# Performance work log

Measured on AMD Instinct MI355X. Metric: run time of the kernel, lower is better.

The kernel has to match this reference:

```python
import jax, jax.numpy as jnp
import numpy as np

N_NODES = 100000


def gcn_conv(x, src, dst, deg_inv_sqrt, W, b):
    # x: [N, Fin], src/dst: [E_total] (self-loops included), W: [Fin, Fout]
    h = x @ W                                  # [N, Fout]
    norm = deg_inv_sqrt[src] * deg_inv_sqrt[dst]  # [E_total]
    msgs = h[src] * norm[:, None]              # [E_total, Fout] gather
    out = jax.ops.segment_sum(msgs, dst, num_segments=N_NODES)  # scatter-add
    return out + b


def setup_inputs() -> dict:
    key = jax.random.key(0)
    k1, k2, k3, k4, k5, k6, k7, k8 = jax.random.split(key, 8)
    input_dim, hidden_dim, out_dim = 4, 64, 2
    n_edges = 3200000
    x = jax.random.normal(k1, (N_NODES, input_dim), dtype=jnp.float32)
    edge_index = jax.random.randint(k2, (2, n_edges), 0, N_NODES, dtype=jnp.int64)
    s1 = 1.0 / np.sqrt(input_dim)
    s2 = 1.0 / np.sqrt(hidden_dim)
    W1 = jax.random.uniform(k3, (input_dim, hidden_dim), jnp.float32, -s1, s1)
    b1 = jnp.zeros((hidden_dim,), jnp.float32)
    W2 = jax.random.uniform(k4, (hidden_dim, hidden_dim), jnp.float32, -s2, s2)
    b2 = jnp.zeros((hidden_dim,), jnp.float32)
    Wf = jax.random.uniform(k5, (hidden_dim, out_dim), jnp.float32, -s2, s2)
    bf = jax.random.uniform(k6, (out_dim,), jnp.float32, -s2, s2)
    return {"x": x, "edge_index": edge_index, "W1": W1, "b1": b1,
            "W2": W2, "b2": b2, "Wf": Wf, "bf": bf}


def reference(x, edge_index, W1, b1, W2, b2, Wf, bf):
    # Add self-loops (PyG GCNConv default)
    loop = jnp.arange(N_NODES, dtype=edge_index.dtype)
    src = jnp.concatenate([edge_index[0], loop])
    dst = jnp.concatenate([edge_index[1], loop])
    # Symmetric normalization: degree on destination after self-loops
    deg = jax.ops.segment_sum(jnp.ones_like(dst, dtype=x.dtype), dst,
                              num_segments=N_NODES)
    deg_inv_sqrt = jnp.where(deg > 0, jax.lax.rsqrt(deg), 0.0)
    h = jax.nn.relu(gcn_conv(x, src, dst, deg_inv_sqrt, W1, b1))
    h = jax.nn.relu(gcn_conv(h, src, dst, deg_inv_sqrt, W2, b2))
    return h @ Wf + bf
```

## Files before the change

kernel.cpp:

```cpp
#include <hip/hip_runtime.h>
#include <hip/hip_bf16.h>

#define N_NODES 100000
#define N_EDGES 3200000
#define NB ((N_NODES + 255) / 256)
#define NBUCKET NB
#define EPB 8192
#define NPB ((N_EDGES + EPB - 1) / EPB)
#define BCAP 11264

__device__ inline unsigned f2bf(float f) {
  unsigned x = __float_as_uint(f);
  return (x + 0x7FFFu + ((x >> 16) & 1u)) >> 16;
}


__global__ void __launch_bounds__(256) k_pass1(const int* __restrict__ src,
                                               const int* __restrict__ dst,
                                               int* __restrict__ gcur,
                                               unsigned int* __restrict__ eb) {
  __shared__ int hist[NBUCKET];
  __shared__ int gbase[NBUCKET];
  int tid = threadIdx.x;
  int base = blockIdx.x * EPB;
  int cnt = min(EPB, N_EDGES - base);
  int n4 = cnt >> 2;
  for (int i = tid; i < NBUCKET; i += 256) hist[i] = 0;
  __syncthreads();
  const int4* d4 = (const int4*)(dst + base);
  const int4* s4 = (const int4*)(src + base);
  unsigned mv[32];
  unsigned short mb[32];
#pragma unroll
  for (int k = 0; k < 8; ++k) {
    int i = tid + (k << 8);
    if (i < n4) {
      int4 dv = d4[i];
      int4 sv = s4[i];
      int b0 = dv.x >> 8, b1_ = dv.y >> 8, b2 = dv.z >> 8, b3 = dv.w >> 8;
      unsigned p0 = atomicAdd(&hist[b0], 1);
      unsigned p1 = atomicAdd(&hist[b1_], 1);
      unsigned p2 = atomicAdd(&hist[b2], 1);
      unsigned p3 = atomicAdd(&hist[b3], 1);
      mv[4 * k + 0] = (unsigned)sv.x | ((unsigned)(dv.x & 255) << 17) | (p0 << 25);
      mv[4 * k + 1] = (unsigned)sv.y | ((unsigned)(dv.y & 255) << 17) | (p1 << 25);
      mv[4 * k + 2] = (unsigned)sv.z | ((unsigned)(dv.z & 255) << 17) | (p2 << 25);
      mv[4 * k + 3] = (unsigned)sv.w | ((unsigned)(dv.w & 255) << 17) | (p3 << 25);
      mb[4 * k + 0] = (unsigned short)b0;
      mb[4 * k + 1] = (unsigned short)b1_;
      mb[4 * k + 2] = (unsigned short)b2;
      mb[4 * k + 3] = (unsigned short)b3;
    } else {
      mb[4 * k + 0] = 0xFFFF; mb[4 * k + 1] = 0xFFFF;
      mb[4 * k + 2] = 0xFFFF; mb[4 * k + 3] = 0xFFFF;
    }
  }
  __syncthreads();
  for (int b = tid; b < NBUCKET; b += 256) {
    int h = hist[b];
    gbase[b] = h ? atomicAdd(&gcur[b], h) : 0;
  }
  __syncthreads();
#pragma unroll
  for (int k = 0; k < 32; ++k) {
    if (mb[k] != 0xFFFF) {
      int b = mb[k];
      unsigned v = mv[k];
      unsigned pos = (unsigned)gbase[b] + (v >> 25);
      if (pos < BCAP) eb[(size_t)b * BCAP + pos] = v & 0x01FFFFFFu;
    }
  }
}


__global__ void __launch_bounds__(256) k_part2(unsigned int* __restrict__ eb,
                                               const int* __restrict__ gcur,
                                               int* __restrict__ rs, int* __restrict__ re,
                                               float* __restrict__ dis,
                                               const float4* __restrict__ x4,
                                               float4* __restrict__ xd) {
  __shared__ int hist[256], scn[256], cur[256];
  __shared__ int tot;
  __shared__ unsigned int stage[BCAP];
  int b = blockIdx.x, tid = threadIdx.x;
  int n0 = b << 8;
  int cnt = gcur[b];
  int base = b * BCAP;
  hist[tid] = 0; cur[tid] = 0;
  __syncthreads();
  for (int i = tid; i < cnt; i += 256)
    atomicAdd(&hist[eb[base + i] >> 17], 1);
  __syncthreads();
  int n = n0 + tid;
  int deg = hist[tid];
  int slots = (n < N_NODES) ? ((deg + 1 + 15) & ~15) : 0;
  int x = slots;
  scn[tid] = x;
  __syncthreads();
  for (int off = 1; off < 256; off <<= 1) {
    int t = (tid >= off) ? scn[tid - off] : 0;
    __syncthreads();
    x += t; scn[tid] = x;
    __syncthreads();
  }
  int excl = x - slots;
  if (tid == 255) tot = x;
  if (n < N_NODES) {
    rs[n]  = base + excl;
    re[n]  = base + excl + deg + 1;
    float dn = rsqrtf((float)(deg + 1));
    dis[n] = dn;
    float4 xv = x4[n];
    float4 w; w.x = xv.x * dn; w.y = xv.y * dn; w.z = xv.z * dn; w.w = xv.w * dn;
    xd[n] = w;
    stage[excl] = (unsigned)n;
    for (int i = deg + 1; i < slots; ++i)
      stage[excl + i] = (unsigned)N_NODES;
  }
  if (b == 0 && tid == 0) xd[N_NODES] = make_float4(0.f, 0.f, 0.f, 0.f);
  scn[tid] = excl + 1;
  __syncthreads();
  for (int i = tid; i < cnt; i += 256) {
    unsigned v = eb[base + i];
    unsigned low = v >> 17;
    int lpos = scn[low] + atomicAdd(&cur[low], 1);
    stage[lpos] = v & 0x1FFFFu;
  }
  __syncthreads();
  int total = tot;
  for (int i = tid; i < total; i += 256)
    eb[base + i] = stage[i];
  if (tid < 32) {
    int gp = total + tid;
    if (gp < BCAP) eb[base + gp] = (unsigned)N_NODES;
  }
}


__global__ void __launch_bounds__(256) k_l1(const float4* __restrict__ xd,
                                            const float* __restrict__ dis,
                                            const int* __restrict__ rs,
                                            const int* __restrict__ re,
                                            const int* __restrict__ csr,
                                            const float* __restrict__ W1,
                                            const float* __restrict__ b1,
                                            unsigned int* __restrict__ h1o) {
  int gt = blockIdx.x * 256 + threadIdx.x;
  int nid = gt >> 2, p = gt & 3;
  if (nid > N_NODES) return;
  if (nid == N_NODES) {
    uint4 z = make_uint4(0u, 0u, 0u, 0u);
    uint4* op = (uint4*)(h1o + nid * 32 + p * 8);
    op[0] = z; op[1] = z;
    return;
  }
  int e0 = rs[nid];
  int nbk = (re[nid] - e0 + 15) >> 4;
  const int4* cp = (const int4*)(csr + e0) + p;
  float ax = 0.f, ay = 0.f, az = 0.f, aw = 0.f;
  for (int t = 0; t < nbk; ++t) {
    int4 s4 = cp[t << 2];
    float4 v0 = xd[s4.x];
    float4 v1 = xd[s4.y];
    float4 v2 = xd[s4.z];
    float4 v3 = xd[s4.w];
    ax += (v0.x + v1.x) + (v2.x + v3.x);
    ay += (v0.y + v1.y) + (v2.y + v3.y);
    az += (v0.z + v1.z) + (v2.z + v3.z);
    aw += (v0.w + v1.w) + (v2.w + v3.w);
  }
  ax += __shfl_xor(ax, 1); ax += __shfl_xor(ax, 2);
  ay += __shfl_xor(ay, 1); ay += __shfl_xor(ay, 2);
  az += __shfl_xor(az, 1); az += __shfl_xor(az, 2);
  aw += __shfl_xor(aw, 1); aw += __shfl_xor(aw, 2);
  float dn = dis[nid];
  ax *= dn; ay *= dn; az *= dn; aw *= dn;
  int j0 = p << 4;
  unsigned ou[8];
#pragma unroll
  for (int j2 = 0; j2 < 8; ++j2) {
    int j = j0 + j2 * 2;
    float s0 = b1[j]     + ax * W1[j]     + ay * W1[64 + j]     + az * W1[128 + j]     + aw * W1[192 + j];
    float s1 = b1[j + 1] + ax * W1[j + 1] + ay * W1[64 + j + 1] + az * W1[128 + j + 1] + aw * W1[192 + j + 1];
    unsigned u0 = f2bf(fmaxf(s0, 0.f) * dn);
    unsigned u1 = f2bf(fmaxf(s1, 0.f) * dn);
    ou[j2] = u0 | (u1 << 16);
  }
  uint4* op = (uint4*)(h1o + nid * 32 + p * 8);
  op[0] = make_uint4(ou[0], ou[1], ou[2], ou[3]);
  op[1] = make_uint4(ou[4], ou[5], ou[6], ou[7]);
}


__device__ inline void acc_bf2(float& a0, float& a1, unsigned u) {
  a0 += __uint_as_float(u << 16);
  a1 += __uint_as_float(u & 0xffff0000u);
}

__global__ void __launch_bounds__(256)
k_layer2(const __hip_bfloat16* __restrict__ h1s, const float* __restrict__ dis,
         const int* __restrict__ rs, const int* __restrict__ re,
         const int* __restrict__ csr,
         const float* __restrict__ W2, const float* __restrict__ b2,
         const float* __restrict__ Wf, const float* __restrict__ bf,
         float* __restrict__ out) {
  __shared__ float sh[4][64];
  int l = threadIdx.x & 63;
  int w = threadIdx.x >> 6;
  int n = blockIdx.x * 4 + w;
  int g = l >> 4;
  int c = l & 15;

  const unsigned int* h32 = (const unsigned int*)h1s;
  int e0 = rs[n];
  int iter = (re[n] - e0 + 15) >> 4;
  const int4* cp = (const int4*)(csr + e0) + g;
  int coff = c << 1;

  float4 acc = make_float4(0.f, 0.f, 0.f, 0.f);
  int4 ns = cp[4];
  int4 cs = cp[0];
  uint2 u0 = *(const uint2*)(h32 + (cs.x << 5) + coff);
  uint2 u1 = *(const uint2*)(h32 + (cs.y << 5) + coff);
  uint2 u2 = *(const uint2*)(h32 + (cs.z << 5) + coff);
  uint2 u3 = *(const uint2*)(h32 + (cs.w << 5) + coff);
  for (int it = 1; it < iter; ++it) {
    int4 fs = cp[(it + 1) << 2];
    uint2 n0 = *(const uint2*)(h32 + (ns.x << 5) + coff);
    uint2 n1 = *(const uint2*)(h32 + (ns.y << 5) + coff);
    uint2 n2 = *(const uint2*)(h32 + (ns.z << 5) + coff);
    uint2 n3 = *(const uint2*)(h32 + (ns.w << 5) + coff);
    acc_bf2(acc.x, acc.y, u0.x); acc_bf2(acc.z, acc.w, u0.y);
    acc_bf2(acc.x, acc.y, u1.x); acc_bf2(acc.z, acc.w, u1.y);
    acc_bf2(acc.x, acc.y, u2.x); acc_bf2(acc.z, acc.w, u2.y);
    acc_bf2(acc.x, acc.y, u3.x); acc_bf2(acc.z, acc.w, u3.y);
    u0 = n0; u1 = n1; u2 = n2; u3 = n3;
    ns = fs;
  }
  acc_bf2(acc.x, acc.y, u0.x); acc_bf2(acc.z, acc.w, u0.y);
  acc_bf2(acc.x, acc.y, u1.x); acc_bf2(acc.z, acc.w, u1.y);
  acc_bf2(acc.x, acc.y, u2.x); acc_bf2(acc.z, acc.w, u2.y);
  acc_bf2(acc.x, acc.y, u3.x); acc_bf2(acc.z, acc.w, u3.y);

  acc.x += __shfl_xor(acc.x, 16); acc.x += __shfl_xor(acc.x, 32);
  acc.y += __shfl_xor(acc.y, 16); acc.y += __shfl_xor(acc.y, 32);
  acc.z += __shfl_xor(acc.z, 16); acc.z += __shfl_xor(acc.z, 32);
  acc.w += __shfl_xor(acc.w, 16); acc.w += __shfl_xor(acc.w, 32);

  float dn = dis[n];
  if (l < 16) {
    float4 v; v.x = acc.x * dn; v.y = acc.y * dn; v.z = acc.z * dn; v.w = acc.w * dn;
    *(float4*)&sh[w][c << 2] = v;
  }
  __syncthreads();

  float t = b2[l];
  const float4* shv = (const float4*)sh[w];
#pragma unroll 4
  for (int j4 = 0; j4 < 16; ++j4) {
    float4 a4 = shv[j4];
    t += a4.x * W2[(4 * j4 + 0) * 64 + l];
    t += a4.y * W2[(4 * j4 + 1) * 64 + l];
    t += a4.z * W2[(4 * j4 + 2) * 64 + l];
    t += a4.w * W2[(4 * j4 + 3) * 64 + l];
  }
  t = fmaxf(t, 0.0f);

  float p0 = t * Wf[l * 2 + 0];
  float p1 = t * Wf[l * 2 + 1];
  for (int off = 32; off; off >>= 1) {
    p0 += __shfl_down(p0, off);
    p1 += __shfl_down(p1, off);
  }
  if (l == 0) {
    out[n * 2 + 0] = p0 + bf[0];
    out[n * 2 + 1] = p1 + bf[1];
  }
}


extern "C" void kernel_launch(void* const* d_in, const int* in_sizes, int n_in,
                              void* d_out, int out_size, void* d_ws, size_t ws_size,
                              hipStream_t stream) {
  const float* x  = (const float*)d_in[0];
  const int*   ei = (const int*)d_in[1];
  const float* W1 = (const float*)d_in[2];
  const float* b1 = (const float*)d_in[3];
  const float* W2 = (const float*)d_in[4];
  const float* b2 = (const float*)d_in[5];
  const float* Wf = (const float*)d_in[6];
  const float* bf = (const float*)d_in[7];
  float* out = (float*)d_out;

  const int* srcv = ei;
  const int* dstv = ei + N_EDGES;

  char* p = (char*)d_ws;
  auto take = [&](size_t bytes) { char* r = p; p += (bytes + 255) & ~(size_t)255; return r; };
  int*          gcur = (int*)take((size_t)NBUCKET * 4);
  unsigned int* eb   = (unsigned int*)take((size_t)NBUCKET * BCAP * 4 + 512);
  int*          rs   = (int*)take((size_t)N_NODES * 4);
  int*          re   = (int*)take((size_t)N_NODES * 4);
  float*        dis  = (float*)take((size_t)N_NODES * 4);
  float4*       xd   = (float4*)take((size_t)(N_NODES + 1) * 16);
  __hip_bfloat16* h1s = (__hip_bfloat16*)take((size_t)(N_NODES + 1) * 64 * 2);

  (void)hipMemsetAsync(gcur, 0, (size_t)NBUCKET * 4, stream);
  k_pass1<<<NPB, 256, 0, stream>>>(srcv, dstv, gcur, eb);
  k_part2<<<NBUCKET, 256, 0, stream>>>(eb, gcur, rs, re, dis, (const float4*)x, xd);
  const int* csr = (const int*)eb;
  k_l1<<<((N_NODES + 1) * 4 + 255) / 256, 256, 0, stream>>>(xd, dis, rs, re, csr, W1, b1, (unsigned int*)h1s);
  k_layer2<<<N_NODES / 4, 256, 0, stream>>>(h1s, dis, rs, re, csr, W2, b2, Wf, bf, out);
}
```

Before: 250.5 us.

## Pad CSR rows to 8 and regroup edge gathers into 8 edge lanes

Per-node CSR row padding drops from multiples of 16 to multiples of 8, which cuts the dummy-edge gathers for low-degree nodes. Layer 1 now has each of its 4 lanes take one index per step in a strided pattern instead of int4 chunks. Layer 2 splits the wave into 8 edge groups of 8 lanes, each lane loading 16 bytes (8 bf16 features) per edge, and reduces the groups with a 3-step shuffle. The trade-off is more loop iterations per thread and different coalescing of the index and feature loads.

```diff
diff --git a/kernel.cpp b/kernel.cpp
--- a/kernel.cpp
+++ b/kernel.cpp
@@ -93,7 +93,7 @@
   __syncthreads();
   int n = n0 + tid;
   int deg = hist[tid];
-  int slots = (n < N_NODES) ? ((deg + 1 + 15) & ~15) : 0;
+  int slots = (n < N_NODES) ? ((deg + 1 + 7) & ~7) : 0;
   int x = slots;
   scn[tid] = x;
   __syncthreads();
@@ -130,7 +130,7 @@
   int total = tot;
   for (int i = tid; i < total; i += 256)
     eb[base + i] = stage[i];
-  if (tid < 32) {
+  if (tid < 16) {
     int gp = total + tid;
     if (gp < BCAP) eb[base + gp] = (unsigned)N_NODES;
   }
@@ -155,19 +155,14 @@
     return;
   }
   int e0 = rs[nid];
-  int nbk = (re[nid] - e0 + 15) >> 4;
-  const int4* cp = (const int4*)(csr + e0) + p;
+  int it4 = ((re[nid] - e0 + 7) & ~7) >> 2;
+  const int* cp = csr + e0 + p;
   float ax = 0.f, ay = 0.f, az = 0.f, aw = 0.f;
-  for (int t = 0; t < nbk; ++t) {
-    int4 s4 = cp[t << 2];
-    float4 v0 = xd[s4.x];
-    float4 v1 = xd[s4.y];
-    float4 v2 = xd[s4.z];
-    float4 v3 = xd[s4.w];
-    ax += (v0.x + v1.x) + (v2.x + v3.x);
-    ay += (v0.y + v1.y) + (v2.y + v3.y);
-    az += (v0.z + v1.z) + (v2.z + v3.z);
-    aw += (v0.w + v1.w) + (v2.w + v3.w);
+#pragma unroll 4
+  for (int t = 0; t < it4; ++t) {
+    int s = cp[t << 2];
+    float4 v = xd[s];
+    ax += v.x; ay += v.y; az += v.z; aw += v.w;
   }
   ax += __shfl_xor(ax, 1); ax += __shfl_xor(ax, 2);
   ay += __shfl_xor(ay, 1); ay += __shfl_xor(ay, 2);
@@ -208,49 +203,40 @@
   int l = threadIdx.x & 63;
   int w = threadIdx.x >> 6;
   int n = blockIdx.x * 4 + w;
-  int g = l >> 4;
-  int c = l & 15;
+  int g = l >> 3;
+  int c = l & 7;
 
   const unsigned int* h32 = (const unsigned int*)h1s;
   int e0 = rs[n];
-  int iter = (re[n] - e0 + 15) >> 4;
-  const int4* cp = (const int4*)(csr + e0) + g;
-  int coff = c << 1;
-
-  float4 acc = make_float4(0.f, 0.f, 0.f, 0.f);
-  int4 ns = cp[4];
-  int4 cs = cp[0];
-  uint2 u0 = *(const uint2*)(h32 + (cs.x << 5) + coff);
-  uint2 u1 = *(const uint2*)(h32 + (cs.y << 5) + coff);
-  uint2 u2 = *(const uint2*)(h32 + (cs.z << 5) + coff);
-  uint2 u3 = *(const uint2*)(h32 + (cs.w << 5) + coff);
+  int iter = (re[n] - e0 + 7) >> 3;
+  const int* cb = csr + e0 + g;
+  int coff = c << 2;
+
+  float a0 = 0.f, a1 = 0.f, a2 = 0.f, a3 = 0.f;
+  float a4 = 0.f, a5 = 0.f, a6 = 0.f, a7 = 0.f;
+  int sc = cb[0];
+  int sn = cb[8];
+  uint4 u = *(const uint4*)(h32 + (sc << 5) + coff);
   for (int it = 1; it < iter; ++it) {
-    int4 fs = cp[(it + 1) << 2];
-    uint2 n0 = *(const uint2*)(h32 + (ns.x << 5) + coff);
-    uint2 n1 = *(const uint2*)(h32 + (ns.y << 5) + coff);
-    uint2 n2 = *(const uint2*)(h32 + (ns.z << 5) + coff);
-    uint2 n3 = *(const uint2*)(h32 + (ns.w << 5) + coff);
-    acc_bf2(acc.x, acc.y, u0.x); acc_bf2(acc.z, acc.w, u0.y);
-    acc_bf2(acc.x, acc.y, u1.x); acc_bf2(acc.z, acc.w, u1.y);
-    acc_bf2(acc.x, acc.y, u2.x); acc_bf2(acc.z, acc.w, u2.y);
-    acc_bf2(acc.x, acc.y, u3.x); acc_bf2(acc.z, acc.w, u3.y);
-    u0 = n0; u1 = n1; u2 = n2; u3 = n3;
-    ns = fs;
-  }
-  acc_bf2(acc.x, acc.y, u0.x); acc_bf2(acc.z, acc.w, u0.y);
-  acc_bf2(acc.x, acc.y, u1.x); acc_bf2(acc.z, acc.w, u1.y);
-  acc_bf2(acc.x, acc.y, u2.x); acc_bf2(acc.z, acc.w, u2.y);
-  acc_bf2(acc.x, acc.y, u3.x); acc_bf2(acc.z, acc.w, u3.y);
-
-  acc.x += __shfl_xor(acc.x, 16); acc.x += __shfl_xor(acc.x, 32);
-  acc.y += __shfl_xor(acc.y, 16); acc.y += __shfl_xor(acc.y, 32);
-  acc.z += __shfl_xor(acc.z, 16); acc.z += __shfl_xor(acc.z, 32);
-  acc.w += __shfl_xor(acc.w, 16); acc.w += __shfl_xor(acc.w, 32);
+    int sf = cb[(it + 1) << 3];
+    uint4 r = *(const uint4*)(h32 + (sn << 5) + coff);
+    acc_bf2(a0, a1, u.x); acc_bf2(a2, a3, u.y);
+    acc_bf2(a4, a5, u.z); acc_bf2(a6, a7, u.w);
+    u = r; sn = sf;
+  }
+  acc_bf2(a0, a1, u.x); acc_bf2(a2, a3, u.y);
+  acc_bf2(a4, a5, u.z); acc_bf2(a6, a7, u.w);
+
+#define RED3(a) a += __shfl_xor(a, 8); a += __shfl_xor(a, 16); a += __shfl_xor(a, 32);
+  RED3(a0) RED3(a1) RED3(a2) RED3(a3) RED3(a4) RED3(a5) RED3(a6) RED3(a7)
+#undef RED3
 
   float dn = dis[n];
-  if (l < 16) {
-    float4 v; v.x = acc.x * dn; v.y = acc.y * dn; v.z = acc.z * dn; v.w = acc.w * dn;
-    *(float4*)&sh[w][c << 2] = v;
+  if (l < 8) {
+    float4 v0; v0.x = a0 * dn; v0.y = a1 * dn; v0.z = a2 * dn; v0.w = a3 * dn;
+    float4 v1; v1.x = a4 * dn; v1.y = a5 * dn; v1.z = a6 * dn; v1.w = a7 * dn;
+    *(float4*)&sh[w][(l << 3) + 0] = v0;
+    *(float4*)&sh[w][(l << 3) + 4] = v1;
   }
   __syncthreads();
 
@@ -258,11 +244,11 @@
   const float4* shv = (const float4*)sh[w];
 #pragma unroll 4
   for (int j4 = 0; j4 < 16; ++j4) {
-    float4 a4 = shv[j4];
-    t += a4.x * W2[(4 * j4 + 0) * 64 + l];
-    t += a4.y * W2[(4 * j4 + 1) * 64 + l];
-    t += a4.z * W2[(4 * j4 + 2) * 64 + l];
-    t += a4.w * W2[(4 * j4 + 3) * 64 + l];
+    float4 a4v = shv[j4];
+    t += a4v.x * W2[(4 * j4 + 0) * 64 + l];
+    t += a4v.y * W2[(4 * j4 + 1) * 64 + l];
+    t += a4v.z * W2[(4 * j4 + 2) * 64 + l];
+    t += a4v.w * W2[(4 * j4 + 3) * 64 + l];
   }
   t = fmaxf(t, 0.0f);
 
```

Measured after the change: 246.6 us. No clear change (-1.5%).
